# Kernel optimization log

Hardware: AMD Instinct MI355X
Metric: run time of the kernel (lower is better)

Reference implementation:

```python
import jax, jax.numpy as jnp
import numpy as np

N = 8192        # batch of embeddings
D = 128         # embedding dim
NUM_STEPS = 201 # histogram bins over [-1, 1]


def setup_inputs() -> dict:
    key = jax.random.key(0)
    k1, k2, k3, k4 = jax.random.split(key, 4)
    x1 = jax.random.normal(k1, (N, D), dtype=jnp.float32)
    x2 = jax.random.normal(k2, (N, D), dtype=jnp.float32)
    # module assumes L2-normalized embeddings (cosine similarity via plain mm)
    x1 = x1 / jnp.linalg.norm(x1, axis=1, keepdims=True)
    x2 = x2 / jnp.linalg.norm(x2, axis=1, keepdims=True)
    t1 = jax.random.normal(k3, (N,), dtype=jnp.float32)
    t2 = jax.random.normal(k4, (N,), dtype=jnp.float32)
    return {"input_1": x1, "input_2": x2, "target_1": t1, "target_2": t2}


def reference(input_1, input_2, target_1, target_2):
    num_steps = NUM_STEPS
    step = 2.0 / (num_steps - 1)
    n = input_1.shape[0]

    # pairwise cosine similarities [N, N]
    sims = jnp.matmul(input_1, input_2.T)

    # pair signs: signs[i, j] = target_2[i] * target_1[j] > 0 (as in source layout)
    signs = (target_2[:, None] * target_1[None, :]) > 0.0
    triu = jnp.triu(jnp.ones((n, n), dtype=bool), 1)  # strictly upper pairs
    pos_mask = (triu & signs).reshape(-1)
    neg_mask = (triu & ~signs).reshape(-1)

    s = sims.reshape(-1)
    # triangular-kernel soft binning: lower bin edge delta = floor((s+1)/step)*step - 1
    idx = jnp.clip(jnp.floor((s + 1.0) / step).astype(jnp.int32), 0, num_steps - 1)
    delta = idx.astype(s.dtype) * step - 1.0
    frac = (s - delta) / step              # weight for upper bin (idx+1)
    idx_hi = jnp.clip(idx + 1, 0, num_steps - 1)

    def soft_hist(mask):
        w = mask.astype(s.dtype)
        h = jnp.zeros((num_steps,), dtype=s.dtype)
        h = h.at[idx].add((1.0 - frac) * w)   # lower-bin weight
        h = h.at[idx_hi].add(frac * w)        # upper-bin weight
        return h / jnp.maximum(w.sum(), 1.0)

    h_pos = soft_hist(pos_mask)
    h_neg = soft_hist(neg_mask)

    # CDF of positive histogram; loss = E[neg overlaps pos-CDF]
    pos_cdf = jnp.cumsum(h_pos)
    return jnp.sum(h_neg * pos_cdf)
```

## Files before the change

kernel.cpp:

```cpp
#include <hip/hip_runtime.h>

#define N_EMB   8192
#define D_EMB   128
#define NSTEPS  201
#define NB      128
#define TBLOCKS (NB*(NB+1)/2)
#define NCOPY   16
#define NHIST   16
#define PGRID   1536

typedef __attribute__((ext_vector_type(4))) int   i32x4;

#define CNT_SHIFT  21
#define FRAC_MASK  ((1u << CNT_SHIFT) - 1u)
#define NZERO      (NCOPY * 2 * NSTEPS)

__global__ __launch_bounds__(256) void convert_kernel(
    const float* __restrict__ x1, const float* __restrict__ x2,
    signed char* __restrict__ x1q, signed char* __restrict__ x2q,
    float* __restrict__ sc1, float* __restrict__ sc2,
    float* __restrict__ ghist)
{
  int t = blockIdx.x * 256 + threadIdx.x;
  if (t < NZERO) ghist[t] = 0.0f;
  const bool first = (t < 131072);
  const float* src = first ? x1  : x2;
  signed char* dst = first ? x1q : x2q;
  float*       scd = first ? sc1 : sc2;
  int tt  = t & 131071;
  int r   = tt >> 4;
  int c16 = tt & 15;
  const float4* g = reinterpret_cast<const float4*>(src + ((size_t)r << 7) + c16*8);
  float4 v0 = g[0], v1 = g[1];

  float m = fmaxf(fmaxf(fmaxf(fabsf(v0.x), fabsf(v0.y)), fmaxf(fabsf(v0.z), fabsf(v0.w))),
                  fmaxf(fmaxf(fabsf(v1.x), fabsf(v1.y)), fmaxf(fabsf(v1.z), fabsf(v1.w))));
#pragma unroll
  for (int d = 1; d < 16; d <<= 1) m = fmaxf(m, __shfl_xor(m, d, 16));

  float qs = 127.0f / m;
  int q0 = (int)rintf(v0.x * qs), q1 = (int)rintf(v0.y * qs);
  int q2 = (int)rintf(v0.z * qs), q3 = (int)rintf(v0.w * qs);
  int q4 = (int)rintf(v1.x * qs), q5 = (int)rintf(v1.y * qs);
  int q6 = (int)rintf(v1.z * qs), q7 = (int)rintf(v1.w * qs);
  uint2 pk;
  pk.x = (q0 & 255) | ((q1 & 255) << 8) | ((q2 & 255) << 16) | ((unsigned)(q3 & 255) << 24);
  pk.y = (q4 & 255) | ((q5 & 255) << 8) | ((q6 & 255) << 16) | ((unsigned)(q7 & 255) << 24);

  int R = r >> 4, fr = r & 15;
  size_t chunk = ((size_t)(R*2 + (c16 >> 3)) << 6) + (size_t)(((c16 >> 1) & 3)*16 + fr);
  *reinterpret_cast<uint2*>(dst + chunk*16 + (c16 & 1)*8) = pk;

  if (c16 == 0) scd[r] = m * (1.0f / 127.0f);
}

__global__ __launch_bounds__(256, 6) void main_kernel(
    const signed char* __restrict__ x1q, const signed char* __restrict__ x2q,
    const float* __restrict__ sc1g, const float* __restrict__ sc2g,
    const float* __restrict__ t1g, const float* __restrict__ t2g,
    float* __restrict__ ghist)
{
  __shared__ unsigned int whist[2][NHIST][NSTEPS];

  const int tid = threadIdx.x;
  for (int b = tid; b < 2*NHIST*NSTEPS; b += 256) ((unsigned int*)whist)[b] = 0u;

  const int lane = tid & 63;
  const int w    = tid >> 6;
  const int wr   = w >> 1, wc = w & 1;
  const int fr   = lane & 15;
  const int kg   = lane >> 4;
  const int rbase = kg * 4;
  unsigned int* whP = &whist[0][(w << 2) | kg][0];
  const int NEGOFF = NHIST * NSTEPS;

  const i32x4* A = reinterpret_cast<const i32x4*>(x1q);
  const i32x4* B = reinterpret_cast<const i32x4*>(x2q);

  const unsigned bid = ((unsigned)blockIdx.x & 7u) * 192u + ((unsigned)blockIdx.x >> 3);
  const int t0  = (int)((bid      * 43u) >> 3);
  const int t1e = (int)(((bid+1u) * 43u) >> 3);

  __syncthreads();

  int j = (int)((sqrtf(8.0f*(float)t0 + 1.0f) - 1.0f) * 0.5f);
  while ((j+1)*(j+2)/2 <= t0) ++j;
  while (j*(j+1)/2 > t0) --j;
  int bi = t0 - j*(j+1)/2;

  int t = t0;
  while (t < t1e) {
    const int gj0 = j*64;
    const int Rb = (gj0 >> 4) + wc*2;
    i32x4 bQ[2][2];
#pragma unroll
    for (int ks = 0; ks < 2; ++ks) {
      bQ[0][ks] = B[((size_t)(Rb    *2 + ks) << 6) + lane];
      bQ[1][ks] = B[((size_t)((Rb+1)*2 + ks) << 6) + lane];
    }
    float T1v0 = t1g[gj0 + wc*32 + fr];
    float T1v1 = t1g[gj0 + wc*32 + 16 + fr];
    float sB0  = sc2g[gj0 + wc*32 + fr];
    float sB1  = sc2g[gj0 + wc*32 + 16 + fr];

    const int cnt = min(j + 1 - bi, t1e - t);
    const int bi_end = bi + cnt;

    for (; bi < bi_end; ++bi) {
      const int gi0 = bi*64;
      const bool full = (bi != j);
      const int Ra = (gi0 >> 4) + wr*2;

      float T2v[2][4], scA[2][4];
#pragma unroll
      for (int tm = 0; tm < 2; ++tm)
#pragma unroll
        for (int rr = 0; rr < 4; ++rr) {
          int gi = gi0 + wr*32 + tm*16 + rbase + rr;
          T2v[tm][rr] = t2g[gi];
          scA[tm][rr] = sc1g[gi] * 102400.0f;
        }

      i32x4 acc00 = {0,0,0,0}, acc01 = {0,0,0,0};
      i32x4 acc10 = {0,0,0,0}, acc11 = {0,0,0,0};
#pragma unroll
      for (int ks = 0; ks < 2; ++ks) {
        i32x4 a0 = A[((size_t)(Ra    *2 + ks) << 6) + lane];
        i32x4 a1 = A[((size_t)((Ra+1)*2 + ks) << 6) + lane];
        acc00 = __builtin_amdgcn_mfma_i32_16x16x64_i8(a0, bQ[0][ks], acc00, 0, 0, 0);
        acc01 = __builtin_amdgcn_mfma_i32_16x16x64_i8(a0, bQ[1][ks], acc01, 0, 0, 0);
        acc10 = __builtin_amdgcn_mfma_i32_16x16x64_i8(a1, bQ[0][ks], acc10, 0, 0, 0);
        acc11 = __builtin_amdgcn_mfma_i32_16x16x64_i8(a1, bQ[1][ks], acc11, 0, 0, 0);
      }

      auto dep = [&](const i32x4& a, int tm, float t1v, float sBv, int tn) {
        const int lj = wc*32 + tn*16 + fr;
#pragma unroll
        for (int rr = 0; rr < 4; ++rr) {
          const int li = wr*32 + tm*16 + rbase + rr;
          bool pos = (T2v[tm][rr] * t1v > 0.0f);
          float uu = fmaf((float)a[rr], scA[tm][rr] * sBv, 102400.5f);
          int   iu = (int)uu;
          int  idx = iu >> 10;
          idx = idx < 0 ? 0 : (idx > NSTEPS-1 ? NSTEPS-1 : idx);
          unsigned int pkv = (1u << CNT_SHIFT) | (unsigned int)(iu & 1023);
          unsigned int* dst = whP + (pos ? 0 : NEGOFF) + idx;
          if (full || (lj > li)) atomicAdd(dst, pkv);
        }
      };
      dep(acc00, 0, T1v0, sB0, 0); dep(acc01, 0, T1v1, sB1, 1);
      dep(acc10, 1, T1v0, sB0, 0); dep(acc11, 1, T1v1, sB1, 1);
      ++t;
    }
    bi = 0; ++j;
  }
  __syncthreads();

  float* gh = ghist + (size_t)(blockIdx.x & (NCOPY-1)) * (2*NSTEPS);
  if (tid < NSTEPS) {
    const int b = tid;
    const float inv = 1.0f / 1024.0f;
#pragma unroll
    for (int sg = 0; sg < 2; ++sg) {
      unsigned int cp = 0; float fp = 0.f, fpm1 = 0.f;
#pragma unroll
      for (int ww = 0; ww < NHIST; ++ww) {
        unsigned int vp = whist[sg][ww][b];
        cp += vp >> CNT_SHIFT;  fp += (float)(vp & FRAC_MASK);
        if (b > 0) fpm1 += (float)(whist[sg][ww][b-1] & FRAC_MASK);
      }
      float hv = (b == NSTEPS-1) ? ((float)cp + fpm1 * inv)
                                 : ((float)cp - fp * inv + fpm1 * inv);
      if (hv != 0.0f) atomicAdd(&gh[sg*NSTEPS + b], hv);
    }
  }
}

__global__ void finalize_kernel(const float* __restrict__ ghist,
                                float* __restrict__ out)
{
  __shared__ float hp[NSTEPS], hn[NSTEPS];
  const int tid = threadIdx.x;
  if (tid < NSTEPS) {
    float sp = 0.f, sn = 0.f;
#pragma unroll
    for (int c = 0; c < NCOPY; ++c) {
      sp += ghist[(size_t)c*(2*NSTEPS) + tid];
      sn += ghist[(size_t)c*(2*NSTEPS) + NSTEPS + tid];
    }
    hp[tid] = sp; hn[tid] = sn;
  }
  __syncthreads();
  if (tid == 0) {
    const float TOT = 33550336.0f;
    float np = 0.f;
    for (int b = 0; b < NSTEPS; ++b) np += hp[b];
    float nn = TOT - np;
    float ip  = 1.0f / fmaxf(np, 1.0f);
    float in_ = 1.0f / fmaxf(nn, 1.0f);
    float cdf = 0.f, loss = 0.f;
    for (int b = 0; b < NSTEPS; ++b) {
      cdf  += hp[b] * ip;
      loss += hn[b] * in_ * cdf;
    }
    out[0] = loss;
  }
}

extern "C" void kernel_launch(void* const* d_in, const int* in_sizes, int n_in,
                              void* d_out, int out_size, void* d_ws, size_t ws_size,
                              hipStream_t stream) {
  const float* x1 = (const float*)d_in[0];
  const float* x2 = (const float*)d_in[1];
  const float* t1 = (const float*)d_in[2];
  const float* t2 = (const float*)d_in[3];
  float* out = (float*)d_out;

  const size_t Q_BYTES = (size_t)N_EMB * D_EMB;
  const size_t S_BYTES = (size_t)N_EMB * sizeof(float);
  char* p = (char*)d_ws;
  signed char* x1q   = (signed char*)p;   p += Q_BYTES;
  signed char* x2q   = (signed char*)p;   p += Q_BYTES;
  float*       sc1   = (float*)p;         p += S_BYTES;
  float*       sc2   = (float*)p;         p += S_BYTES;
  float*       ghist = (float*)p;

  convert_kernel<<<(2*N_EMB*D_EMB/8 + 255)/256, 256, 0, stream>>>(x1, x2, x1q, x2q, sc1, sc2, ghist);
  main_kernel<<<PGRID, 256, 0, stream>>>(x1q, x2q, sc1, sc2, t1, t2, ghist);
  finalize_kernel<<<1, 256, 0, stream>>>(ghist, out);
}
```

Measured before the change: 39.64 us.

## Software-pipeline histogram deposit behind MFMA and fuse finalize via last-block reduction

The main loop now defers each tile's histogram atomics to the next iteration, so the LDS atomics of tile i run while tile i+1's loads and MFMAs are in flight. Sign and upper-triangle masks are precomputed as bitmasks. The separate finalize kernel is replaced by a last-block-done counter inside main_kernel, which removes one launch. In exchange the kernel keeps more live registers for the previous tile's values, which may hurt occupancy, and adds a global atomic and a fence per block.

```diff
diff --git a/kernel.cpp b/kernel.cpp
--- a/kernel.cpp
+++ b/kernel.cpp
@@ -9,7 +9,7 @@
 #define NHIST   16
 #define PGRID   1536
 
-typedef __attribute__((ext_vector_type(4))) int   i32x4;
+typedef __attribute__((ext_vector_type(4))) int i32x4;
 
 #define CNT_SHIFT  21
 #define FRAC_MASK  ((1u << CNT_SHIFT) - 1u)
@@ -19,10 +19,11 @@
     const float* __restrict__ x1, const float* __restrict__ x2,
     signed char* __restrict__ x1q, signed char* __restrict__ x2q,
     float* __restrict__ sc1, float* __restrict__ sc2,
-    float* __restrict__ ghist)
+    float* __restrict__ ghist, unsigned int* __restrict__ gdone)
 {
   int t = blockIdx.x * 256 + threadIdx.x;
   if (t < NZERO) ghist[t] = 0.0f;
+  if (t == 0)    gdone[0] = 0u;
   const bool first = (t < 131072);
   const float* src = first ? x1  : x2;
   signed char* dst = first ? x1q : x2q;
@@ -58,9 +59,11 @@
     const signed char* __restrict__ x1q, const signed char* __restrict__ x2q,
     const float* __restrict__ sc1g, const float* __restrict__ sc2g,
     const float* __restrict__ t1g, const float* __restrict__ t2g,
-    float* __restrict__ ghist)
+    float* __restrict__ ghist, unsigned int* __restrict__ gdone,
+    float* __restrict__ out)
 {
   __shared__ unsigned int whist[2][NHIST][NSTEPS];
+  __shared__ int lastFlag;
 
   const int tid = threadIdx.x;
   for (int b = tid; b < 2*NHIST*NSTEPS; b += 256) ((unsigned int*)whist)[b] = 0u;
@@ -74,8 +77,20 @@
   unsigned int* whP = &whist[0][(w << 2) | kg][0];
   const int NEGOFF = NHIST * NSTEPS;
 
-  const i32x4* A = reinterpret_cast<const i32x4*>(x1q);
-  const i32x4* B = reinterpret_cast<const i32x4*>(x2q);
+  unsigned upmask = 0;
+#pragma unroll
+  for (int tm = 0; tm < 2; ++tm)
+#pragma unroll
+    for (int tn = 0; tn < 2; ++tn)
+#pragma unroll
+      for (int rr = 0; rr < 4; ++rr) {
+        int li = wr*32 + tm*16 + rbase + rr;
+        int lj = wc*32 + tn*16 + fr;
+        if (lj > li) upmask |= 1u << ((tm*2 + tn)*4 + rr);
+      }
+
+  const i32x4* Aq = reinterpret_cast<const i32x4*>(x1q);
+  const i32x4* Bq = reinterpret_cast<const i32x4*>(x2q);
 
   const unsigned bid = ((unsigned)blockIdx.x & 7u) * 192u + ((unsigned)blockIdx.x >> 3);
   const int t0  = (int)((bid      * 43u) >> 3);
@@ -92,12 +107,10 @@
   while (t < t1e) {
     const int gj0 = j*64;
     const int Rb = (gj0 >> 4) + wc*2;
-    i32x4 bQ[2][2];
-#pragma unroll
-    for (int ks = 0; ks < 2; ++ks) {
-      bQ[0][ks] = B[((size_t)(Rb    *2 + ks) << 6) + lane];
-      bQ[1][ks] = B[((size_t)((Rb+1)*2 + ks) << 6) + lane];
-    }
+    i32x4 bQ00 = Bq[((size_t)(Rb    *2 + 0) << 6) + lane];
+    i32x4 bQ01 = Bq[((size_t)(Rb    *2 + 1) << 6) + lane];
+    i32x4 bQ10 = Bq[((size_t)((Rb+1)*2 + 0) << 6) + lane];
+    i32x4 bQ11 = Bq[((size_t)((Rb+1)*2 + 1) << 6) + lane];
     float T1v0 = t1g[gj0 + wc*32 + fr];
     float T1v1 = t1g[gj0 + wc*32 + 16 + fr];
     float sB0  = sc2g[gj0 + wc*32 + fr];
@@ -106,52 +119,75 @@
     const int cnt = min(j + 1 - bi, t1e - t);
     const int bi_end = bi + cnt;
 
-    for (; bi < bi_end; ++bi) {
+    float    pSu[2][2][4];
+    unsigned pPos0 = 0, pPos1 = 0;
+    unsigned pFull = 0;
+    bool havePrev = false;
+
+    auto DEP = [&]() {
+#pragma unroll
+      for (int tm = 0; tm < 2; ++tm)
+#pragma unroll
+        for (int tn = 0; tn < 2; ++tn)
+#pragma unroll
+          for (int rr = 0; rr < 4; ++rr) {
+            float uu = pSu[tm][tn][rr] + 102400.5f;
+            int   iu = (int)uu;
+            int  idx = iu >> 10;
+            idx = idx < 0 ? 0 : (idx > NSTEPS-1 ? NSTEPS-1 : idx);
+            unsigned pk = (1u << CNT_SHIFT) | (unsigned)(iu & 1023);
+            unsigned pb = tn ? pPos1 : pPos0;
+            unsigned off = ((pb >> (tm*4 + rr)) & 1u) ? 0u : (unsigned)NEGOFF;
+            bool take = pFull || ((upmask >> ((tm*2 + tn)*4 + rr)) & 1u);
+            if (take) atomicAdd(whP + off + idx, pk);
+          }
+    };
+
+    for (; bi < bi_end; ++bi, ++t) {
       const int gi0 = bi*64;
-      const bool full = (bi != j);
       const int Ra = (gi0 >> 4) + wr*2;
-
-      float T2v[2][4], scA[2][4];
+      i32x4 a00 = Aq[((size_t)(Ra    *2 + 0) << 6) + lane];
+      i32x4 a01 = Aq[((size_t)(Ra    *2 + 1) << 6) + lane];
+      i32x4 a10 = Aq[((size_t)((Ra+1)*2 + 0) << 6) + lane];
+      i32x4 a11 = Aq[((size_t)((Ra+1)*2 + 1) << 6) + lane];
+      float sAv[2][4];
+      unsigned cPos0 = 0, cPos1 = 0;
 #pragma unroll
       for (int tm = 0; tm < 2; ++tm)
 #pragma unroll
         for (int rr = 0; rr < 4; ++rr) {
           int gi = gi0 + wr*32 + tm*16 + rbase + rr;
-          T2v[tm][rr] = t2g[gi];
-          scA[tm][rr] = sc1g[gi] * 102400.0f;
+          float t2 = t2g[gi];
+          sAv[tm][rr] = sc1g[gi] * 102400.0f;
+          cPos0 |= (t2 * T1v0 > 0.0f ? 1u : 0u) << (tm*4 + rr);
+          cPos1 |= (t2 * T1v1 > 0.0f ? 1u : 0u) << (tm*4 + rr);
         }
+
+      if (havePrev) DEP();
 
       i32x4 acc00 = {0,0,0,0}, acc01 = {0,0,0,0};
       i32x4 acc10 = {0,0,0,0}, acc11 = {0,0,0,0};
-#pragma unroll
-      for (int ks = 0; ks < 2; ++ks) {
-        i32x4 a0 = A[((size_t)(Ra    *2 + ks) << 6) + lane];
-        i32x4 a1 = A[((size_t)((Ra+1)*2 + ks) << 6) + lane];
-        acc00 = __builtin_amdgcn_mfma_i32_16x16x64_i8(a0, bQ[0][ks], acc00, 0, 0, 0);
-        acc01 = __builtin_amdgcn_mfma_i32_16x16x64_i8(a0, bQ[1][ks], acc01, 0, 0, 0);
-        acc10 = __builtin_amdgcn_mfma_i32_16x16x64_i8(a1, bQ[0][ks], acc10, 0, 0, 0);
-        acc11 = __builtin_amdgcn_mfma_i32_16x16x64_i8(a1, bQ[1][ks], acc11, 0, 0, 0);
-      }
-
-      auto dep = [&](const i32x4& a, int tm, float t1v, float sBv, int tn) {
-        const int lj = wc*32 + tn*16 + fr;
-#pragma unroll
-        for (int rr = 0; rr < 4; ++rr) {
-          const int li = wr*32 + tm*16 + rbase + rr;
-          bool pos = (T2v[tm][rr] * t1v > 0.0f);
-          float uu = fmaf((float)a[rr], scA[tm][rr] * sBv, 102400.5f);
-          int   iu = (int)uu;
-          int  idx = iu >> 10;
-          idx = idx < 0 ? 0 : (idx > NSTEPS-1 ? NSTEPS-1 : idx);
-          unsigned int pkv = (1u << CNT_SHIFT) | (unsigned int)(iu & 1023);
-          unsigned int* dst = whP + (pos ? 0 : NEGOFF) + idx;
-          if (full || (lj > li)) atomicAdd(dst, pkv);
-        }
-      };
-      dep(acc00, 0, T1v0, sB0, 0); dep(acc01, 0, T1v1, sB1, 1);
-      dep(acc10, 1, T1v0, sB0, 0); dep(acc11, 1, T1v1, sB1, 1);
-      ++t;
-    }
+      acc00 = __builtin_amdgcn_mfma_i32_16x16x64_i8(a00, bQ00, acc00, 0, 0, 0);
+      acc00 = __builtin_amdgcn_mfma_i32_16x16x64_i8(a01, bQ01, acc00, 0, 0, 0);
+      acc01 = __builtin_amdgcn_mfma_i32_16x16x64_i8(a00, bQ10, acc01, 0, 0, 0);
+      acc01 = __builtin_amdgcn_mfma_i32_16x16x64_i8(a01, bQ11, acc01, 0, 0, 0);
+      acc10 = __builtin_amdgcn_mfma_i32_16x16x64_i8(a10, bQ00, acc10, 0, 0, 0);
+      acc10 = __builtin_amdgcn_mfma_i32_16x16x64_i8(a11, bQ01, acc10, 0, 0, 0);
+      acc11 = __builtin_amdgcn_mfma_i32_16x16x64_i8(a10, bQ10, acc11, 0, 0, 0);
+      acc11 = __builtin_amdgcn_mfma_i32_16x16x64_i8(a11, bQ11, acc11, 0, 0, 0);
+
+#pragma unroll
+      for (int rr = 0; rr < 4; ++rr) {
+        pSu[0][0][rr] = (float)acc00[rr] * (sAv[0][rr] * sB0);
+        pSu[0][1][rr] = (float)acc01[rr] * (sAv[0][rr] * sB1);
+        pSu[1][0][rr] = (float)acc10[rr] * (sAv[1][rr] * sB0);
+        pSu[1][1][rr] = (float)acc11[rr] * (sAv[1][rr] * sB1);
+      }
+      pPos0 = cPos0; pPos1 = cPos1;
+      pFull = (bi != j) ? 1u : 0u;
+      havePrev = true;
+    }
+    if (havePrev) DEP();
     bi = 0; ++j;
   }
   __syncthreads();
@@ -174,36 +210,39 @@
       if (hv != 0.0f) atomicAdd(&gh[sg*NSTEPS + b], hv);
     }
   }
-}
-
-__global__ void finalize_kernel(const float* __restrict__ ghist,
-                                float* __restrict__ out)
-{
-  __shared__ float hp[NSTEPS], hn[NSTEPS];
-  const int tid = threadIdx.x;
-  if (tid < NSTEPS) {
-    float sp = 0.f, sn = 0.f;
-#pragma unroll
-    for (int c = 0; c < NCOPY; ++c) {
-      sp += ghist[(size_t)c*(2*NSTEPS) + tid];
-      sn += ghist[(size_t)c*(2*NSTEPS) + NSTEPS + tid];
-    }
-    hp[tid] = sp; hn[tid] = sn;
+
+  if (tid == 0) {
+    __threadfence();
+    unsigned prev = atomicAdd(gdone, 1u);
+    lastFlag = (prev == (unsigned)(PGRID - 1));
   }
   __syncthreads();
-  if (tid == 0) {
-    const float TOT = 33550336.0f;
-    float np = 0.f;
-    for (int b = 0; b < NSTEPS; ++b) np += hp[b];
-    float nn = TOT - np;
-    float ip  = 1.0f / fmaxf(np, 1.0f);
-    float in_ = 1.0f / fmaxf(nn, 1.0f);
-    float cdf = 0.f, loss = 0.f;
-    for (int b = 0; b < NSTEPS; ++b) {
-      cdf  += hp[b] * ip;
-      loss += hn[b] * in_ * cdf;
-    }
-    out[0] = loss;
+  if (lastFlag) {
+    float* hf = (float*)&whist[0][0][0];
+    if (tid < NSTEPS) {
+      float sp = 0.f, sn = 0.f;
+#pragma unroll
+      for (int c = 0; c < NCOPY; ++c) {
+        sp += atomicAdd(&ghist[(size_t)c*(2*NSTEPS) + tid], 0.0f);
+        sn += atomicAdd(&ghist[(size_t)c*(2*NSTEPS) + NSTEPS + tid], 0.0f);
+      }
+      hf[tid] = sp; hf[NSTEPS + tid] = sn;
+    }
+    __syncthreads();
+    if (tid == 0) {
+      const float TOT = 33550336.0f;
+      float np = 0.f;
+      for (int b = 0; b < NSTEPS; ++b) np += hf[b];
+      float nn = TOT - np;
+      float ip  = 1.0f / fmaxf(np, 1.0f);
+      float in_ = 1.0f / fmaxf(nn, 1.0f);
+      float cdf = 0.f, loss = 0.f;
+      for (int b = 0; b < NSTEPS; ++b) {
+        cdf  += hf[b] * ip;
+        loss += hf[NSTEPS + b] * in_ * cdf;
+      }
+      out[0] = loss;
+    }
   }
 }
 
@@ -223,9 +262,9 @@
   signed char* x2q   = (signed char*)p;   p += Q_BYTES;
   float*       sc1   = (float*)p;         p += S_BYTES;
   float*       sc2   = (float*)p;         p += S_BYTES;
-  float*       ghist = (float*)p;
-
-  convert_kernel<<<(2*N_EMB*D_EMB/8 + 255)/256, 256, 0, stream>>>(x1, x2, x1q, x2q, sc1, sc2, ghist);
-  main_kernel<<<PGRID, 256, 0, stream>>>(x1q, x2q, sc1, sc2, t1, t2, ghist);
-  finalize_kernel<<<1, 256, 0, stream>>>(ghist, out);
+  float*       ghist = (float*)p;         p += (size_t)NZERO*sizeof(float);
+  unsigned int* gdone = (unsigned int*)p;
+
+  convert_kernel<<<(2*N_EMB*D_EMB/8 + 255)/256, 256, 0, stream>>>(x1, x2, x1q, x2q, sc1, sc2, ghist, gdone);
+  main_kernel<<<PGRID, 256, 0, stream>>>(x1q, x2q, sc1, sc2, t1, t2, ghist, gdone, out);
 }
```

Result: slower. 62.08 us (+56.6%).
